# Kernel optimization log

Measured on AMD Instinct MI355X. Metric: run time of the kernel, lower is better.

## Reference

```python
import jax, jax.numpy as jnp
import numpy as np

# YOLOv4 stride-8 head config (yolov4.cfg)
ALL_ANCHORS = [[12,16],[19,36],[40,28],[36,75],[76,55],[72,146],[142,110],[192,243],[459,401]]
ANCHOR_MASK = [0, 1, 2]
N_CLASSES = 80
SCALE_XY = 1.2  # scale_x_y for this head
N_BBOX_ATTRS = 5  # tx, ty, tw, th, obj


def setup_inputs() -> dict:
    key = jax.random.key(0)
    attrs = N_CLASSES + N_BBOX_ATTRS  # 85
    n_anchors = len(ANCHOR_MASK)      # 3
    # raw conv output: [batch, n_anchors*attrs, grid, grid]
    x = jax.random.normal(key, (16, n_anchors * attrs, 76, 76), dtype=jnp.float32)
    return {"x": x, "input_dim": 608}


def reference(x, input_dim):
    B = x.shape[0]
    G = x.shape[2]                      # grid_dim (INPUT_H_DIM)
    stride = input_dim // G             # grid_stride
    A = len(ANCHOR_MASK)
    attrs = N_CLASSES + N_BBOX_ATTRS

    # anchors scaled to grid units: [A, 2]
    anc = jnp.asarray([ALL_ANCHORS[i] for i in ANCHOR_MASK], dtype=jnp.float32) / stride

    # [B, A, attrs, H, W] -> [B, H, W, A, attrs]
    x = x.reshape(B, A, attrs, G, G).transpose(0, 3, 4, 1, 2)

    # yolo_transform: sigmoid+scale tx/ty, exp*anchor tw/th, sigmoid obj+cls
    txy = jax.nn.sigmoid(x[..., 0:2]) * SCALE_XY - (SCALE_XY - 1.0) / 2.0
    twh = jnp.exp(x[..., 2:4]) * anc            # broadcast over [B,H,W,A,2]
    objcls = jax.nn.sigmoid(x[..., 4:])

    # add_grid_offsets: torch.meshgrid(grid, grid) is 'ij' -> y_offset[i,j]=i, x_offset[i,j]=j
    gy, gx = jnp.meshgrid(jnp.arange(G), jnp.arange(G), indexing="ij")
    off = jnp.stack([gx, gy], axis=-1).astype(jnp.float32)[:, :, None, :]  # [H,W,1,2]
    txy = txy + off

    # scale bbox attrs (tx..th) to input-image pixels
    boxes = jnp.concatenate([txy, twh], axis=-1) * jnp.float32(stride)

    out = jnp.concatenate([boxes, objcls], axis=-1)  # [B,H,W,A,attrs]
    return out.reshape(B, G * G * A, attrs)
```

## Files before the change

kernel.cpp:

```cpp
#include <hip/hip_runtime.h>

#define GRIDD  76
#define NROWS  255
#define GG     (GRIDD * GRIDD)
#define UROWS  128
#define UPITCH 76
#define UDW    (UROWS * UPITCH)

typedef __attribute__((address_space(3))) unsigned lds_u32;
typedef __attribute__((address_space(1))) unsigned glb_u32;

__device__ __forceinline__ void gll16(const float* g, float* l) {
    __builtin_amdgcn_global_load_lds((const glb_u32*)g, (lds_u32*)l, 16, 0, 0);
}

__global__ __launch_bounds__(512, 8) void yolo_head_kernel(
    const float* __restrict__ x, const int* __restrict__ dimp,
    float* __restrict__ out)
{
    __shared__ float buf[UDW];
    const unsigned lb   = (blockIdx.x & 7u) * 304u + (blockIdx.x >> 3);
    const unsigned b    = lb / (GRIDD * 2);
    const unsigned hr   = lb - b * (GRIDD * 2);
    const unsigned h    = hr >> 1;
    const unsigned rbase = (hr & 1u) * 127u;
    const unsigned t    = threadIdx.x;
    const unsigned wid  = t >> 6;
    const unsigned lane = t & 63u;
    const float stride  = (float)(*dimp / GRIDD);
    const float mB      = -0.1f * stride;

    const float* __restrict__ src = x + (size_t)b * (NROWS * GG)
                                      + (size_t)rbase * GG + (size_t)h * GRIDD;
    #pragma unroll
    for (unsigned k = 0; k < 5u; ++k) {
        unsigned i = k * 512u + (wid << 6) + lane;
        if (i < 2432u) {
            unsigned row = i / 19u;
            unsigned c4  = (i - row * 19u) << 2;
            gll16(src + (size_t)row * GG + c4,
                  buf + (size_t)(k * 512u + (wid << 6)) * 4u);
        }
    }
    __syncthreads();

    const float fh = (float)h;
    float* __restrict__ outbh = out + (size_t)(b * GRIDD + h) * (GRIDD * NROWS);

    #pragma unroll
    for (unsigned j = 0; j < 5u; ++j) {
        unsigned tt = wid + (j << 3);
        if (tt < 38u) {
            const unsigned rc  = tt & 1u;
            const unsigned wc  = tt >> 1;
            const unsigned r   = (rc << 6) + lane;
            const unsigned rem = rbase + r;
            const unsigned a    = (rem >= 170u) ? 2u : ((rem >= 85u) ? 1u : 0u);
            const unsigned attr = rem - a * 85u;
            const bool  wh  = (attr == 2u) | (attr == 3u);
            const bool  isx = (attr == 0u);
            float anc = 0.f;
            if (attr == 2u) anc = (a == 0u) ? 12.f : ((a == 1u) ? 19.f : 40.f);
            if (attr == 3u) anc = (a == 0u) ? 16.f : ((a == 1u) ? 36.f : 28.f);
            const float sgn = wh ? 1.f : -1.f;
            const float A   = (attr < 2u) ? 1.2f * stride : 1.f;
            const float B0  = (attr == 1u) ? (fh * stride + mB) : 0.f;

            const float4 vv = *reinterpret_cast<const float4*>(&buf[r * UPITCH + (wc << 2)]);
            float* __restrict__ dst = outbh + rem;
            #pragma unroll
            for (unsigned i = 0; i < 4u; ++i) {
                const float v = (i == 0) ? vv.x : (i == 1) ? vv.y : (i == 2) ? vv.z : vv.w;
                const float w = (float)((wc << 2) + i);
                const float e = __expf(sgn * v);
                const float sig = __builtin_amdgcn_rcpf(1.0f + e);
                const float Bi  = isx ? fmaf(w, stride, mB) : B0;
                const float o   = wh ? e * anc : fmaf(sig, A, Bi);
                dst[(size_t)((wc << 2) + i) * NROWS] = o;
            }
        }
    }
}

extern "C" void kernel_launch(void* const* d_in, const int* in_sizes, int n_in,
                              void* d_out, int out_size, void* d_ws, size_t ws_size,
                              hipStream_t stream) {
    const float* x  = (const float*)d_in[0];
    const int* dimp = (const int*)d_in[1];
    float* out      = (float*)d_out;
    const int B = in_sizes[0] / (NROWS * GG);
    yolo_head_kernel<<<B * GRIDD * 2, 512, 0, stream>>>(x, dimp, out);
}
```

Measured before the change: 33.10 us.

## Give each wavefront a private 16-row LDS slab and drop block barrier

Each of the 8 wavefronts now loads its own 16 channel rows into a private LDS region and waits only on its own vmcnt instead of a block-wide __syncthreads. The per-lane attribute decode is hoisted out of the loop, since each lane now owns one fixed channel row and walks columns. Store patterns change: each instruction now writes 16 consecutive channels across 4 columns instead of 64 consecutive channels. The risk is narrower store coalescing. Relying on vmcnt alone for LDS-direct loads, without a barrier, may also need careful ordering.

```diff
diff --git a/kernel.cpp b/kernel.cpp
--- a/kernel.cpp
+++ b/kernel.cpp
@@ -3,9 +3,9 @@
 #define GRIDD  76
 #define NROWS  255
 #define GG     (GRIDD * GRIDD)
-#define UROWS  128
-#define UPITCH 76
-#define UDW    (UROWS * UPITCH)
+#define WR     16
+#define WQ     (WR * 19)
+#define WDW    (WR * GRIDD)
 
 typedef __attribute__((address_space(3))) unsigned lds_u32;
 typedef __attribute__((address_space(1))) unsigned glb_u32;
@@ -18,65 +18,62 @@
     const float* __restrict__ x, const int* __restrict__ dimp,
     float* __restrict__ out)
 {
-    __shared__ float buf[UDW];
-    const unsigned lb   = (blockIdx.x & 7u) * 304u + (blockIdx.x >> 3);
-    const unsigned b    = lb / (GRIDD * 2);
-    const unsigned hr   = lb - b * (GRIDD * 2);
-    const unsigned h    = hr >> 1;
+    __shared__ float buf[8 * WDW];
+    const unsigned lb    = (blockIdx.x & 7u) * 304u + (blockIdx.x >> 3);
+    const unsigned b     = lb / 152u;
+    const unsigned hr    = lb - b * 152u;
+    const unsigned h     = hr >> 1;
     const unsigned rbase = (hr & 1u) * 127u;
-    const unsigned t    = threadIdx.x;
-    const unsigned wid  = t >> 6;
-    const unsigned lane = t & 63u;
-    const float stride  = (float)(*dimp / GRIDD);
-    const float mB      = -0.1f * stride;
+    const unsigned t     = threadIdx.x;
+    const unsigned W     = t >> 6;
+    const unsigned lane  = t & 63u;
+    const float stride   = (float)(*dimp / GRIDD);
+    const float mB       = -0.1f * stride;
 
-    const float* __restrict__ src = x + (size_t)b * (NROWS * GG)
-                                      + (size_t)rbase * GG + (size_t)h * GRIDD;
+    float* wbuf = buf + W * WDW;
+    const unsigned wr0 = rbase + W * WR;
+    const float* __restrict__ src = x + (size_t)(b * NROWS + wr0) * GG + h * GRIDD;
     #pragma unroll
     for (unsigned k = 0; k < 5u; ++k) {
-        unsigned i = k * 512u + (wid << 6) + lane;
-        if (i < 2432u) {
+        unsigned i = k * 64u + lane;
+        if (i < WQ) {
             unsigned row = i / 19u;
-            unsigned c4  = (i - row * 19u) << 2;
-            gll16(src + (size_t)row * GG + c4,
-                  buf + (size_t)(k * 512u + (wid << 6)) * 4u);
+            unsigned qc  = i - row * 19u;
+            gll16(src + (size_t)row * GG + (qc << 2), wbuf + k * 256u);
         }
     }
-    __syncthreads();
+    asm volatile("s_waitcnt vmcnt(0)" ::: "memory");
 
-    const float fh = (float)h;
-    float* __restrict__ outbh = out + (size_t)(b * GRIDD + h) * (GRIDD * NROWS);
+    const unsigned r    = lane & 15u;
+    const unsigned rem  = wr0 + r;
+    const unsigned a    = (rem >= 170u) ? 2u : ((rem >= 85u) ? 1u : 0u);
+    const unsigned attr = rem - a * 85u;
+    const bool  wh  = (attr == 2u) | (attr == 3u);
+    const bool  isx = (attr == 0u);
+    float anc = 0.f;
+    if (attr == 2u) anc = (a == 0u) ? 12.f : ((a == 1u) ? 19.f : 40.f);
+    if (attr == 3u) anc = (a == 0u) ? 16.f : ((a == 1u) ? 36.f : 28.f);
+    const float sgn = wh ? 1.f : -1.f;
+    const float A   = (attr < 2u) ? 1.2f * stride : 1.f;
+    const float B0  = (attr == 1u) ? ((float)h * stride + mB) : 0.f;
+
+    const float* lr = wbuf + r * GRIDD;
+    float* __restrict__ dst = out + (size_t)(b * GRIDD + h) * (GRIDD * NROWS) + rem;
 
     #pragma unroll
     for (unsigned j = 0; j < 5u; ++j) {
-        unsigned tt = wid + (j << 3);
-        if (tt < 38u) {
-            const unsigned rc  = tt & 1u;
-            const unsigned wc  = tt >> 1;
-            const unsigned r   = (rc << 6) + lane;
-            const unsigned rem = rbase + r;
-            const unsigned a    = (rem >= 170u) ? 2u : ((rem >= 85u) ? 1u : 0u);
-            const unsigned attr = rem - a * 85u;
-            const bool  wh  = (attr == 2u) | (attr == 3u);
-            const bool  isx = (attr == 0u);
-            float anc = 0.f;
-            if (attr == 2u) anc = (a == 0u) ? 12.f : ((a == 1u) ? 19.f : 40.f);
-            if (attr == 3u) anc = (a == 0u) ? 16.f : ((a == 1u) ? 36.f : 28.f);
-            const float sgn = wh ? 1.f : -1.f;
-            const float A   = (attr < 2u) ? 1.2f * stride : 1.f;
-            const float B0  = (attr == 1u) ? (fh * stride + mB) : 0.f;
-
-            const float4 vv = *reinterpret_cast<const float4*>(&buf[r * UPITCH + (wc << 2)]);
-            float* __restrict__ dst = outbh + rem;
+        const unsigned qj = (lane >> 4) + (j << 2);
+        if (qj < 19u) {
+            const float4 vv = *reinterpret_cast<const float4*>(lr + (qj << 2));
             #pragma unroll
             for (unsigned i = 0; i < 4u; ++i) {
                 const float v = (i == 0) ? vv.x : (i == 1) ? vv.y : (i == 2) ? vv.z : vv.w;
-                const float w = (float)((wc << 2) + i);
-                const float e = __expf(sgn * v);
+                const unsigned u = (qj << 2) + i;
+                const float e   = __expf(sgn * v);
                 const float sig = __builtin_amdgcn_rcpf(1.0f + e);
-                const float Bi  = isx ? fmaf(w, stride, mB) : B0;
+                const float Bi  = isx ? fmaf((float)u, stride, mB) : B0;
                 const float o   = wh ? e * anc : fmaf(sig, A, Bi);
-                dst[(size_t)((wc << 2) + i) * NROWS] = o;
+                dst[(size_t)u * NROWS] = o;
             }
         }
     }
```

Result: slower. 34.06 us (+2.9%).
